# Optimization experiments

Hardware: AMD Instinct MI355X
Metric: run time of the kernel (lower is better)

## Reference

```python
import jax, jax.numpy as jnp
import numpy as np

EPS = 1e-6

def setup_inputs() -> dict:
    key = jax.random.key(0)
    k1, k2, k3, k4, k5 = jax.random.split(key, 5)
    B, Lq, Lk, D, Dc = 8, 1024, 8192, 256, 128
    q = jax.random.normal(k1, (B, Lq, D), dtype=jnp.float32)
    k_q = jax.random.randint(k2, (B, Lk, Dc), 0, 16, dtype=jnp.int32)  # 4-bit codes
    k_scale = jax.random.uniform(k3, (B, 1, Dc), dtype=jnp.float32)
    k_zero = jax.random.uniform(k4, (B, 1, Dc), dtype=jnp.float32) * 15.0
    W_up = jax.random.normal(k5, (D, Dc), dtype=jnp.float32) / np.sqrt(Dc)
    return {"q": q, "k_q": k_q, "k_scale": k_scale, "k_zero": k_zero, "W_up": W_up}

def reference(q, k_q, k_scale, k_zero, W_up):
    # int4 dequantization: (B, Lk, Dc)
    k_c = k_scale * (k_q.astype(jnp.float32) - k_zero)
    # low-rank decompress (nn.Linear(d_compressed, d_model, bias=False)): k = k_c @ W_up.T -> (B, Lk, D)
    k = jnp.einsum('blc,dc->bld', k_c, W_up)
    # squared norms (raw values used in diff, clamped values used in denominator)
    q_sq = jnp.sum(q * q, axis=-1)  # (B, Lq)
    k_sq = jnp.sum(k * k, axis=-1)  # (B, Lk)
    q_norm_sq = jnp.minimum(q_sq, 1.0 - EPS)
    k_norm_sq = jnp.minimum(k_sq, 1.0 - EPS)
    # ||q_i - k_j||^2 via expansion (same math as materializing the diff tensor)
    qk = jnp.einsum('bqd,bkd->bqk', q, k)  # (B, Lq, Lk)
    diff_norm_sq = jnp.maximum(q_sq[:, :, None] + k_sq[:, None, :] - 2.0 * qk, 0.0)
    denom = (1.0 - q_norm_sq)[:, :, None] * (1.0 - k_norm_sq)[:, None, :] + EPS
    dist = jnp.arccosh(1.0 + 2.0 * diff_norm_sq / denom)  # (B, Lq, Lk)
    return dist
```

## Files before the change

kernel.cpp:

```cpp
#include <hip/hip_runtime.h>
#include <hip/hip_bf16.h>

#define B_   8
#define LQ   1024
#define LK   8192
#define D_   256
#define DC   128
#define EPSF 1e-6f

typedef __attribute__((ext_vector_type(8))) short short8;
typedef __attribute__((ext_vector_type(4))) float floatx4;

static __device__ __forceinline__ floatx4 mfma16(short8 a, short8 b, floatx4 c) {
    return __builtin_amdgcn_mfma_f32_16x16x32_bf16(a, b, c, 0, 0, 0);
}

__global__ void k_G(const float* __restrict__ W, __hip_bfloat16* __restrict__ G) {
    int c1 = blockIdx.x, c2 = threadIdx.x;
    float acc = 0.f;
    for (int d = 0; d < D_; ++d)
        acc += W[d * DC + c1] * W[d * DC + c2];
    G[c1 * DC + c2] = __float2bfloat16(acc);
}

__global__ __launch_bounds__(256) void k_qsq(const float* __restrict__ q,
                                             float* __restrict__ q_sq) {
    int row  = blockIdx.x * 4 + (threadIdx.x >> 6);
    int lane = threadIdx.x & 63;
    const float* r = q + (size_t)row * D_;
    float s = 0.f;
    for (int i = lane; i < D_; i += 64) { float v = r[i]; s += v * v; }
    for (int m = 1; m < 64; m <<= 1) s += __shfl_xor(s, m);
    if (lane == 0) q_sq[row] = s;
}

__global__ __launch_bounds__(256) void k_qproj(const float* __restrict__ q,
                                               const float* __restrict__ W,
                                               __hip_bfloat16* __restrict__ qproj) {
    __shared__ __hip_bfloat16 sA[128 * 72];
    __shared__ __hip_bfloat16 sB[128 * 72];
    int t = threadIdx.x, lane = t & 63, w = t >> 6;
    int quad = lane >> 4, li = lane & 15;
    int row0 = blockIdx.x * 128;

    floatx4 acc[2][8];
    for (int mt = 0; mt < 2; ++mt)
        for (int nt = 0; nt < 8; ++nt)
            acc[mt][nt] = (floatx4){0.f, 0.f, 0.f, 0.f};

    for (int kc4 = 0; kc4 < 4; ++kc4) {
        for (int it = 0; it < 8; ++it) {
            int idx = it * 256 + t;
            int r = idx >> 4, pos = idx & 15;
            float4 v = *(const float4*)(q + (size_t)(row0 + r) * D_ + kc4 * 64 + pos * 4);
            __hip_bfloat16* dst = &sA[r * 72 + pos * 4];
            dst[0] = __float2bfloat16(v.x); dst[1] = __float2bfloat16(v.y);
            dst[2] = __float2bfloat16(v.z); dst[3] = __float2bfloat16(v.w);
        }
        for (int it = 0; it < 32; ++it) {
            int e = it * 256 + t;
            int dl = e >> 7, c = e & 127;
            sB[c * 72 + dl] = __float2bfloat16(W[(size_t)(kc4 * 64 + dl) * DC + c]);
        }
        __syncthreads();
        short8 af[2][2];
        for (int mt = 0; mt < 2; ++mt)
            for (int ks = 0; ks < 2; ++ks)
                af[mt][ks] = *(const short8*)&sA[(w * 32 + mt * 16 + li) * 72 + ks * 32 + quad * 8];
        for (int nt = 0; nt < 8; ++nt) {
            for (int ks = 0; ks < 2; ++ks) {
                short8 bf = *(const short8*)&sB[(nt * 16 + li) * 72 + ks * 32 + quad * 8];
                acc[0][nt] = mfma16(af[0][ks], bf, acc[0][nt]);
                acc[1][nt] = mfma16(af[1][ks], bf, acc[1][nt]);
            }
        }
        __syncthreads();
    }
    for (int mt = 0; mt < 2; ++mt)
        for (int nt = 0; nt < 8; ++nt)
            for (int r = 0; r < 4; ++r) {
                int row = w * 32 + mt * 16 + quad * 4 + r;
                int c   = nt * 16 + li;
                qproj[(size_t)(row0 + row) * DC + c] = __float2bfloat16(acc[mt][nt][r]);
            }
}

__global__ __launch_bounds__(256) void k_dequant(const int* __restrict__ kq,
                                                 const float* __restrict__ kscale,
                                                 const float* __restrict__ kzero,
                                                 __hip_bfloat16* __restrict__ kc) {
    int i = (blockIdx.x * 256 + threadIdx.x) * 4;
    int4 codes = *(const int4*)(kq + i);
    int c = i & (DC - 1);
    int b = i >> 20;
    float4 sc = *(const float4*)(kscale + b * DC + c);
    float4 zp = *(const float4*)(kzero + b * DC + c);
    __hip_bfloat16* o = kc + i;
    o[0] = __float2bfloat16(sc.x * ((float)codes.x - zp.x));
    o[1] = __float2bfloat16(sc.y * ((float)codes.y - zp.y));
    o[2] = __float2bfloat16(sc.z * ((float)codes.z - zp.z));
    o[3] = __float2bfloat16(sc.w * ((float)codes.w - zp.w));
}

__global__ __launch_bounds__(256) void k_ksq(const __hip_bfloat16* __restrict__ kc,
                                             const __hip_bfloat16* __restrict__ G,
                                             float* __restrict__ k_sq) {
    __shared__ __hip_bfloat16 sK[128 * 128];
    __shared__ __hip_bfloat16 sG[128 * 128];
    int t = threadIdx.x, lane = t & 63, w = t >> 6;
    int quad = lane >> 4, li = lane & 15;
    int b = blockIdx.x >> 6, l0 = (blockIdx.x & 63) * 128;
    const uint4* Ks = (const uint4*)(kc + ((size_t)b * LK + l0) * DC);
    const uint4* Gs = (const uint4*)G;
    uint4* dK = (uint4*)sK; uint4* dG = (uint4*)sG;
    for (int it = 0; it < 8; ++it) {
        int idx = it * 256 + t;
        dK[idx] = Ks[idx];
        dG[idx] = Gs[idx];
    }
    __syncthreads();
    short8 af[2][4];
    for (int mt = 0; mt < 2; ++mt)
        for (int ks = 0; ks < 4; ++ks)
            af[mt][ks] = *(const short8*)&sK[(w * 32 + mt * 16 + li) * DC + ks * 32 + quad * 8];
    float s[2][4] = {{0,0,0,0},{0,0,0,0}};
    for (int nt = 0; nt < 8; ++nt) {
        floatx4 a0 = (floatx4){0.f,0.f,0.f,0.f};
        floatx4 a1 = (floatx4){0.f,0.f,0.f,0.f};
        for (int ks = 0; ks < 4; ++ks) {
            short8 bf = *(const short8*)&sG[(nt * 16 + li) * DC + ks * 32 + quad * 8];
            a0 = mfma16(af[0][ks], bf, a0);
            a1 = mfma16(af[1][ks], bf, a1);
        }
        int c2 = nt * 16 + li;
        for (int r = 0; r < 4; ++r) {
            int r0 = w * 32 +        quad * 4 + r;
            int r1 = w * 32 + 16 +   quad * 4 + r;
            s[0][r] += a0[r] * __bfloat162float(sK[r0 * DC + c2]);
            s[1][r] += a1[r] * __bfloat162float(sK[r1 * DC + c2]);
        }
    }
    for (int mt = 0; mt < 2; ++mt)
        for (int r = 0; r < 4; ++r) {
            float v = s[mt][r];
            v += __shfl_xor(v, 1); v += __shfl_xor(v, 2);
            v += __shfl_xor(v, 4); v += __shfl_xor(v, 8);
            if (li == 0)
                k_sq[(size_t)b * LK + l0 + w * 32 + mt * 16 + quad * 4 + r] = v;
        }
}

__global__ __launch_bounds__(256) void k_main(const __hip_bfloat16* __restrict__ qproj,
                                              const __hip_bfloat16* __restrict__ kc,
                                              const float* __restrict__ q_sq,
                                              const float* __restrict__ k_sq,
                                              float* __restrict__ out) {
    __shared__ __hip_bfloat16 sA[128 * 72];
    __shared__ __hip_bfloat16 sB[128 * 72];
    int t = threadIdx.x, lane = t & 63, w = t >> 6;
    int quad = lane >> 4, li = lane & 15;
    int wm = w >> 1, wn = w & 1;
    int n0 = blockIdx.x * 128, m0 = blockIdx.y * 128, b = blockIdx.z;
    const uint4* Ag = (const uint4*)(qproj + ((size_t)b * LQ + m0) * DC);
    const uint4* Bg = (const uint4*)(kc   + ((size_t)b * LK + n0) * DC);
    uint4* dA = (uint4*)sA; uint4* dB = (uint4*)sB;

    floatx4 acc[4][4];
    for (int i = 0; i < 4; ++i)
        for (int j = 0; j < 4; ++j)
            acc[i][j] = (floatx4){0.f, 0.f, 0.f, 0.f};

    for (int h = 0; h < 2; ++h) {
        for (int it = 0; it < 4; ++it) {
            int idx = it * 256 + t;
            int r = idx >> 3, ch = idx & 7;
            dA[r * 9 + ch] = Ag[r * 16 + h * 8 + ch];
            dB[r * 9 + ch] = Bg[r * 16 + h * 8 + ch];
        }
        __syncthreads();
        for (int ks = 0; ks < 2; ++ks) {
            short8 af[4], bfr[4];
            for (int i = 0; i < 4; ++i) {
                af[i]  = *(const short8*)&sA[(wm * 64 + i * 16 + li) * 72 + ks * 32 + quad * 8];
                bfr[i] = *(const short8*)&sB[(wn * 64 + i * 16 + li) * 72 + ks * 32 + quad * 8];
            }
            for (int i = 0; i < 4; ++i)
                for (int j = 0; j < 4; ++j)
                    acc[i][j] = mfma16(af[i], bfr[j], acc[i][j]);
        }
        __syncthreads();
    }

    float ksv[4], knv[4];
    for (int j = 0; j < 4; ++j) {
        ksv[j] = k_sq[(size_t)b * LK + n0 + wn * 64 + j * 16 + li];
        knv[j] = 1.f - fminf(ksv[j], 1.f - EPSF);
    }
    for (int i = 0; i < 4; ++i) {
        for (int r = 0; r < 4; ++r) {
            int mrow = m0 + wm * 64 + i * 16 + quad * 4 + r;
            size_t gm = (size_t)b * LQ + mrow;
            float qs  = q_sq[gm];
            float omq = 1.f - fminf(qs, 1.f - EPSF);
            float* orow = out + gm * LK + n0 + wn * 64;
            for (int j = 0; j < 4; ++j) {
                float diff  = fmaxf(qs + ksv[j] - 2.f * acc[i][j][r], 0.f);
                float denom = omq * knv[j] + EPSF;
                float delta = (2.f * diff) / denom;
                float dist  = __logf((1.f + delta) + sqrtf(delta * (delta + 2.f)));
                orow[j * 16 + li] = dist;
            }
        }
    }
}

extern "C" void kernel_launch(void* const* d_in, const int* in_sizes, int n_in,
                              void* d_out, int out_size, void* d_ws, size_t ws_size,
                              hipStream_t stream) {
    const float* q      = (const float*)d_in[0];
    const int*   kq     = (const int*)d_in[1];
    const float* kscale = (const float*)d_in[2];
    const float* kzero  = (const float*)d_in[3];
    const float* W      = (const float*)d_in[4];
    float* out = (float*)d_out;

    char* ws = (char*)d_ws;
    __hip_bfloat16* qproj = (__hip_bfloat16*)(ws);
    __hip_bfloat16* kc    = (__hip_bfloat16*)(ws + 2097152);
    __hip_bfloat16* G     = (__hip_bfloat16*)(ws + 18874368);
    float*          q_sq  = (float*)(ws + 18907136);
    float*          k_sq  = (float*)(ws + 18939904);

    k_G      <<<128, 128, 0, stream>>>(W, G);
    k_qsq    <<<2048, 256, 0, stream>>>(q, q_sq);
    k_qproj  <<<64, 256, 0, stream>>>(q, W, qproj);
    k_dequant<<<8192, 256, 0, stream>>>(kq, kscale, kzero, kc);
    k_ksq    <<<512, 256, 0, stream>>>(kc, G, k_sq);
    dim3 grid(LK / 128, LQ / 128, B_);
    k_main   <<<grid, 256, 0, stream>>>(qproj, kc, q_sq, k_sq, out);
}
```

Baseline: 414.3 us.

## Fuse dequant with k-norm, prefetch second K-half, use fast math intrinsics

```diff
diff --git a/kernel.cpp b/kernel.cpp
--- a/kernel.cpp
+++ b/kernel.cpp
@@ -14,22 +14,29 @@
 static __device__ __forceinline__ floatx4 mfma16(short8 a, short8 b, floatx4 c) {
     return __builtin_amdgcn_mfma_f32_16x16x32_bf16(a, b, c, 0, 0, 0);
 }
+static __device__ __forceinline__ float fast_rcp(float x)  { return __builtin_amdgcn_rcpf(x); }
+static __device__ __forceinline__ float fast_sqrt(float x) { return __builtin_amdgcn_sqrtf(x); }
+static __device__ __forceinline__ float fast_ln(float x)   { return 0.69314718056f * __builtin_amdgcn_logf(x); }
 
 __global__ void k_G(const float* __restrict__ W, __hip_bfloat16* __restrict__ G) {
     int c1 = blockIdx.x, c2 = threadIdx.x;
-    float acc = 0.f;
-    for (int d = 0; d < D_; ++d)
-        acc += W[d * DC + c1] * W[d * DC + c2];
-    G[c1 * DC + c2] = __float2bfloat16(acc);
+    float a0 = 0.f, a1 = 0.f, a2 = 0.f, a3 = 0.f;
+#pragma unroll 4
+    for (int d = 0; d < D_; d += 4) {
+        a0 += W[(d + 0) * DC + c1] * W[(d + 0) * DC + c2];
+        a1 += W[(d + 1) * DC + c1] * W[(d + 1) * DC + c2];
+        a2 += W[(d + 2) * DC + c1] * W[(d + 2) * DC + c2];
+        a3 += W[(d + 3) * DC + c1] * W[(d + 3) * DC + c2];
+    }
+    G[c1 * DC + c2] = __float2bfloat16((a0 + a1) + (a2 + a3));
 }
 
 __global__ __launch_bounds__(256) void k_qsq(const float* __restrict__ q,
                                              float* __restrict__ q_sq) {
     int row  = blockIdx.x * 4 + (threadIdx.x >> 6);
     int lane = threadIdx.x & 63;
-    const float* r = q + (size_t)row * D_;
-    float s = 0.f;
-    for (int i = lane; i < D_; i += 64) { float v = r[i]; s += v * v; }
+    float4 v = *(const float4*)(q + (size_t)row * D_ + lane * 4);
+    float s = v.x * v.x + v.y * v.y + v.z * v.z + v.w * v.w;
     for (int m = 1; m < 64; m <<= 1) s += __shfl_xor(s, m);
     if (lane == 0) q_sq[row] = s;
 }
@@ -37,19 +44,19 @@
 __global__ __launch_bounds__(256) void k_qproj(const float* __restrict__ q,
                                                const float* __restrict__ W,
                                                __hip_bfloat16* __restrict__ qproj) {
-    __shared__ __hip_bfloat16 sA[128 * 72];
+    __shared__ __hip_bfloat16 sA[64 * 72];
     __shared__ __hip_bfloat16 sB[128 * 72];
     int t = threadIdx.x, lane = t & 63, w = t >> 6;
     int quad = lane >> 4, li = lane & 15;
-    int row0 = blockIdx.x * 128;
-
-    floatx4 acc[2][8];
-    for (int mt = 0; mt < 2; ++mt)
-        for (int nt = 0; nt < 8; ++nt)
-            acc[mt][nt] = (floatx4){0.f, 0.f, 0.f, 0.f};
+    int row0 = blockIdx.x * 64;
+
+    floatx4 acc[8];
+#pragma unroll
+    for (int nt = 0; nt < 8; ++nt) acc[nt] = (floatx4){0.f, 0.f, 0.f, 0.f};
 
     for (int kc4 = 0; kc4 < 4; ++kc4) {
-        for (int it = 0; it < 8; ++it) {
+#pragma unroll
+        for (int it = 0; it < 4; ++it) {
             int idx = it * 256 + t;
             int r = idx >> 4, pos = idx & 15;
             float4 v = *(const float4*)(q + (size_t)(row0 + r) * D_ + kc4 * 64 + pos * 4);
@@ -57,90 +64,95 @@
             dst[0] = __float2bfloat16(v.x); dst[1] = __float2bfloat16(v.y);
             dst[2] = __float2bfloat16(v.z); dst[3] = __float2bfloat16(v.w);
         }
+#pragma unroll
         for (int it = 0; it < 32; ++it) {
             int e = it * 256 + t;
             int dl = e >> 7, c = e & 127;
             sB[c * 72 + dl] = __float2bfloat16(W[(size_t)(kc4 * 64 + dl) * DC + c]);
         }
         __syncthreads();
-        short8 af[2][2];
-        for (int mt = 0; mt < 2; ++mt)
-            for (int ks = 0; ks < 2; ++ks)
-                af[mt][ks] = *(const short8*)&sA[(w * 32 + mt * 16 + li) * 72 + ks * 32 + quad * 8];
-        for (int nt = 0; nt < 8; ++nt) {
+        short8 af[2];
+#pragma unroll
+        for (int ks = 0; ks < 2; ++ks)
+            af[ks] = *(const short8*)&sA[(w * 16 + li) * 72 + ks * 32 + quad * 8];
+#pragma unroll
+        for (int nt = 0; nt < 8; ++nt)
+#pragma unroll
             for (int ks = 0; ks < 2; ++ks) {
                 short8 bf = *(const short8*)&sB[(nt * 16 + li) * 72 + ks * 32 + quad * 8];
-                acc[0][nt] = mfma16(af[0][ks], bf, acc[0][nt]);
-                acc[1][nt] = mfma16(af[1][ks], bf, acc[1][nt]);
+                acc[nt] = mfma16(af[ks], bf, acc[nt]);
             }
-        }
         __syncthreads();
     }
-    for (int mt = 0; mt < 2; ++mt)
-        for (int nt = 0; nt < 8; ++nt)
-            for (int r = 0; r < 4; ++r) {
-                int row = w * 32 + mt * 16 + quad * 4 + r;
-                int c   = nt * 16 + li;
-                qproj[(size_t)(row0 + row) * DC + c] = __float2bfloat16(acc[mt][nt][r]);
-            }
-}
-
-__global__ __launch_bounds__(256) void k_dequant(const int* __restrict__ kq,
-                                                 const float* __restrict__ kscale,
-                                                 const float* __restrict__ kzero,
-                                                 __hip_bfloat16* __restrict__ kc) {
-    int i = (blockIdx.x * 256 + threadIdx.x) * 4;
-    int4 codes = *(const int4*)(kq + i);
-    int c = i & (DC - 1);
-    int b = i >> 20;
-    float4 sc = *(const float4*)(kscale + b * DC + c);
-    float4 zp = *(const float4*)(kzero + b * DC + c);
-    __hip_bfloat16* o = kc + i;
-    o[0] = __float2bfloat16(sc.x * ((float)codes.x - zp.x));
-    o[1] = __float2bfloat16(sc.y * ((float)codes.y - zp.y));
-    o[2] = __float2bfloat16(sc.z * ((float)codes.z - zp.z));
-    o[3] = __float2bfloat16(sc.w * ((float)codes.w - zp.w));
-}
-
-__global__ __launch_bounds__(256) void k_ksq(const __hip_bfloat16* __restrict__ kc,
-                                             const __hip_bfloat16* __restrict__ G,
-                                             float* __restrict__ k_sq) {
-    __shared__ __hip_bfloat16 sK[128 * 128];
-    __shared__ __hip_bfloat16 sG[128 * 128];
+#pragma unroll
+    for (int nt = 0; nt < 8; ++nt)
+#pragma unroll
+        for (int r = 0; r < 4; ++r) {
+            int row = w * 16 + quad * 4 + r;
+            qproj[(size_t)(row0 + row) * DC + nt * 16 + li] = __float2bfloat16(acc[nt][r]);
+        }
+}
+
+__global__ __launch_bounds__(256) void k_dq_ksq(const int* __restrict__ kq,
+                                                const float* __restrict__ kscale,
+                                                const float* __restrict__ kzero,
+                                                const __hip_bfloat16* __restrict__ G,
+                                                __hip_bfloat16* __restrict__ kc,
+                                                float* __restrict__ k_sq) {
+    __shared__ __hip_bfloat16 sK[128 * 132];
     int t = threadIdx.x, lane = t & 63, w = t >> 6;
     int quad = lane >> 4, li = lane & 15;
     int b = blockIdx.x >> 6, l0 = (blockIdx.x & 63) * 128;
-    const uint4* Ks = (const uint4*)(kc + ((size_t)b * LK + l0) * DC);
-    const uint4* Gs = (const uint4*)G;
-    uint4* dK = (uint4*)sK; uint4* dG = (uint4*)sG;
-    for (int it = 0; it < 8; ++it) {
+
+    const int4* codes = (const int4*)(kq + ((size_t)b * LK + l0) * DC);
+    int col = (t & 31) * 4;
+    float4 sc = *(const float4*)(kscale + b * DC + col);
+    float4 zp = *(const float4*)(kzero + b * DC + col);
+    __hip_bfloat16* kco = kc + ((size_t)b * LK + l0) * DC;
+#pragma unroll
+    for (int it = 0; it < 16; ++it) {
         int idx = it * 256 + t;
-        dK[idx] = Ks[idx];
-        dG[idx] = Gs[idx];
-    }
-    __syncthreads();
+        int r = idx >> 5;
+        int4 c4 = codes[idx];
+        __hip_bfloat16 tmp[4];
+        tmp[0] = __float2bfloat16(sc.x * ((float)c4.x - zp.x));
+        tmp[1] = __float2bfloat16(sc.y * ((float)c4.y - zp.y));
+        tmp[2] = __float2bfloat16(sc.z * ((float)c4.z - zp.z));
+        tmp[3] = __float2bfloat16(sc.w * ((float)c4.w - zp.w));
+        *(uint2*)&sK[r * 132 + col] = *(const uint2*)tmp;
+        *(uint2*)(kco + idx * 4)    = *(const uint2*)tmp;
+    }
+    __syncthreads();
+
     short8 af[2][4];
+#pragma unroll
     for (int mt = 0; mt < 2; ++mt)
+#pragma unroll
         for (int ks = 0; ks < 4; ++ks)
-            af[mt][ks] = *(const short8*)&sK[(w * 32 + mt * 16 + li) * DC + ks * 32 + quad * 8];
-    float s[2][4] = {{0,0,0,0},{0,0,0,0}};
+            af[mt][ks] = *(const short8*)&sK[(w * 32 + mt * 16 + li) * 132 + ks * 32 + quad * 8];
+    float s[2][4] = {{0, 0, 0, 0}, {0, 0, 0, 0}};
+#pragma unroll
     for (int nt = 0; nt < 8; ++nt) {
-        floatx4 a0 = (floatx4){0.f,0.f,0.f,0.f};
-        floatx4 a1 = (floatx4){0.f,0.f,0.f,0.f};
+        floatx4 a0 = (floatx4){0.f, 0.f, 0.f, 0.f};
+        floatx4 a1 = (floatx4){0.f, 0.f, 0.f, 0.f};
+#pragma unroll
         for (int ks = 0; ks < 4; ++ks) {
-            short8 bf = *(const short8*)&sG[(nt * 16 + li) * DC + ks * 32 + quad * 8];
+            short8 bf = *(const short8*)(G + (size_t)(nt * 16 + li) * DC + ks * 32 + quad * 8);
             a0 = mfma16(af[0][ks], bf, a0);
             a1 = mfma16(af[1][ks], bf, a1);
         }
         int c2 = nt * 16 + li;
-        for (int r = 0; r < 4; ++r) {
-            int r0 = w * 32 +        quad * 4 + r;
-            int r1 = w * 32 + 16 +   quad * 4 + r;
-            s[0][r] += a0[r] * __bfloat162float(sK[r0 * DC + c2]);
-            s[1][r] += a1[r] * __bfloat162float(sK[r1 * DC + c2]);
-        }
-    }
+#pragma unroll
+        for (int r = 0; r < 4; ++r) {
+            int r0 = w * 32 +      quad * 4 + r;
+            int r1 = w * 32 + 16 + quad * 4 + r;
+            s[0][r] += a0[r] * __bfloat162float(sK[r0 * 132 + c2]);
+            s[1][r] += a1[r] * __bfloat162float(sK[r1 * 132 + c2]);
+        }
+    }
+#pragma unroll
     for (int mt = 0; mt < 2; ++mt)
+#pragma unroll
         for (int r = 0; r < 4; ++r) {
             float v = s[mt][r];
             v += __shfl_xor(v, 1); v += __shfl_xor(v, 2);
@@ -166,49 +178,87 @@
     uint4* dA = (uint4*)sA; uint4* dB = (uint4*)sB;
 
     floatx4 acc[4][4];
+#pragma unroll
     for (int i = 0; i < 4; ++i)
+#pragma unroll
         for (int j = 0; j < 4; ++j)
             acc[i][j] = (floatx4){0.f, 0.f, 0.f, 0.f};
 
-    for (int h = 0; h < 2; ++h) {
-        for (int it = 0; it < 4; ++it) {
-            int idx = it * 256 + t;
-            int r = idx >> 3, ch = idx & 7;
-            dA[r * 9 + ch] = Ag[r * 16 + h * 8 + ch];
-            dB[r * 9 + ch] = Bg[r * 16 + h * 8 + ch];
-        }
-        __syncthreads();
-        for (int ks = 0; ks < 2; ++ks) {
-            short8 af[4], bfr[4];
-            for (int i = 0; i < 4; ++i) {
-                af[i]  = *(const short8*)&sA[(wm * 64 + i * 16 + li) * 72 + ks * 32 + quad * 8];
-                bfr[i] = *(const short8*)&sB[(wn * 64 + i * 16 + li) * 72 + ks * 32 + quad * 8];
-            }
-            for (int i = 0; i < 4; ++i)
-                for (int j = 0; j < 4; ++j)
-                    acc[i][j] = mfma16(af[i], bfr[j], acc[i][j]);
-        }
-        __syncthreads();
+    int r_ = t >> 3, ch_ = t & 7;
+    uint4 ra[4], rb[4];
+#pragma unroll
+    for (int it = 0; it < 4; ++it) {
+        ra[it] = Ag[(it * 32 + r_) * 16 + ch_];
+        rb[it] = Bg[(it * 32 + r_) * 16 + ch_];
+    }
+#pragma unroll
+    for (int it = 0; it < 4; ++it) {
+        dA[(it * 32 + r_) * 9 + ch_] = ra[it];
+        dB[(it * 32 + r_) * 9 + ch_] = rb[it];
+    }
+    __syncthreads();
+#pragma unroll
+    for (int it = 0; it < 4; ++it) {
+        ra[it] = Ag[(it * 32 + r_) * 16 + 8 + ch_];
+        rb[it] = Bg[(it * 32 + r_) * 16 + 8 + ch_];
+    }
+#pragma unroll
+    for (int ks = 0; ks < 2; ++ks) {
+        short8 af[4], bfr[4];
+#pragma unroll
+        for (int i = 0; i < 4; ++i) {
+            af[i]  = *(const short8*)&sA[(wm * 64 + i * 16 + li) * 72 + ks * 32 + quad * 8];
+            bfr[i] = *(const short8*)&sB[(wn * 64 + i * 16 + li) * 72 + ks * 32 + quad * 8];
+        }
+#pragma unroll
+        for (int i = 0; i < 4; ++i)
+#pragma unroll
+            for (int j = 0; j < 4; ++j)
+                acc[i][j] = mfma16(af[i], bfr[j], acc[i][j]);
+    }
+    __syncthreads();
+#pragma unroll
+    for (int it = 0; it < 4; ++it) {
+        dA[(it * 32 + r_) * 9 + ch_] = ra[it];
+        dB[(it * 32 + r_) * 9 + ch_] = rb[it];
+    }
+    __syncthreads();
+#pragma unroll
+    for (int ks = 0; ks < 2; ++ks) {
+        short8 af[4], bfr[4];
+#pragma unroll
+        for (int i = 0; i < 4; ++i) {
+            af[i]  = *(const short8*)&sA[(wm * 64 + i * 16 + li) * 72 + ks * 32 + quad * 8];
+            bfr[i] = *(const short8*)&sB[(wn * 64 + i * 16 + li) * 72 + ks * 32 + quad * 8];
+        }
+#pragma unroll
+        for (int i = 0; i < 4; ++i)
+#pragma unroll
+            for (int j = 0; j < 4; ++j)
+                acc[i][j] = mfma16(af[i], bfr[j], acc[i][j]);
     }
 
     float ksv[4], knv[4];
+#pragma unroll
     for (int j = 0; j < 4; ++j) {
         ksv[j] = k_sq[(size_t)b * LK + n0 + wn * 64 + j * 16 + li];
         knv[j] = 1.f - fminf(ksv[j], 1.f - EPSF);
     }
+#pragma unroll
     for (int i = 0; i < 4; ++i) {
+#pragma unroll
         for (int r = 0; r < 4; ++r) {
             int mrow = m0 + wm * 64 + i * 16 + quad * 4 + r;
             size_t gm = (size_t)b * LQ + mrow;
             float qs  = q_sq[gm];
             float omq = 1.f - fminf(qs, 1.f - EPSF);
             float* orow = out + gm * LK + n0 + wn * 64;
+#pragma unroll
             for (int j = 0; j < 4; ++j) {
                 float diff  = fmaxf(qs + ksv[j] - 2.f * acc[i][j][r], 0.f);
-                float denom = omq * knv[j] + EPSF;
-                float delta = (2.f * diff) / denom;
-                float dist  = __logf((1.f + delta) + sqrtf(delta * (delta + 2.f)));
-                orow[j * 16 + li] = dist;
+                float delta = 2.f * diff * fast_rcp(omq * knv[j] + EPSF);
+                float sq    = fast_sqrt(delta * (delta + 2.f));
+                orow[j * 16 + li] = fast_ln(1.f + delta + sq);
             }
         }
     }
@@ -231,11 +281,10 @@
     float*          q_sq  = (float*)(ws + 18907136);
     float*          k_sq  = (float*)(ws + 18939904);
 
-    k_G      <<<128, 128, 0, stream>>>(W, G);
-    k_qsq    <<<2048, 256, 0, stream>>>(q, q_sq);
-    k_qproj  <<<64, 256, 0, stream>>>(q, W, qproj);
-    k_dequant<<<8192, 256, 0, stream>>>(kq, kscale, kzero, kc);
-    k_ksq    <<<512, 256, 0, stream>>>(kc, G, k_sq);
+    k_G     <<<128, 128, 0, stream>>>(W, G);
+    k_qsq   <<<2048, 256, 0, stream>>>(q, q_sq);
+    k_qproj <<<128, 256, 0, stream>>>(q, W, qproj);
+    k_dq_ksq<<<512, 256, 0, stream>>>(kq, kscale, kzero, G, kc, k_sq);
     dim3 grid(LK / 128, LQ / 128, B_);
-    k_main   <<<grid, 256, 0, stream>>>(qproj, kc, q_sq, k_sq, out);
-}
+    k_main  <<<grid, 256, 0, stream>>>(qproj, kc, q_sq, k_sq, out);
+}
```

New measurement: 408.5 us. About the same (-1.4%).
